# Kernel optimization log

Measured on AMD Instinct MI355X. Metric: run time of the kernel, lower is better.

## Reference

```python
import jax, jax.numpy as jnp
import numpy as np

N_NODES = 50000
N_EDGES = 800000
IN_FEAT = 128
INTER_DIM = 128
OUT_FEAT = 128
EDGE_W_DIM = 3


def setup_inputs() -> dict:
    key = jax.random.key(0)
    ks = jax.random.split(key, 8)
    h = jax.random.normal(ks[0], (N_NODES, IN_FEAT), dtype=jnp.float32)
    edge_src = jax.random.randint(ks[1], (N_EDGES,), 0, N_NODES, dtype=jnp.int32)
    edge_dst = jax.random.randint(ks[2], (N_EDGES,), 0, N_NODES, dtype=jnp.int32)
    edge_w = jax.random.normal(ks[3], (N_EDGES, EDGE_W_DIM), dtype=jnp.float32)
    # xavier-normal-ish init, gain for relu
    gain = float(np.sqrt(2.0))
    W1 = jax.random.normal(ks[4], (INTER_DIM, IN_FEAT + EDGE_W_DIM), dtype=jnp.float32)
    W1 = W1 * (gain * np.sqrt(2.0 / (INTER_DIM + IN_FEAT + EDGE_W_DIM)))
    b1 = jnp.zeros((INTER_DIM,), dtype=jnp.float32)
    W2 = jax.random.normal(ks[5], (OUT_FEAT, IN_FEAT + INTER_DIM), dtype=jnp.float32)
    W2 = W2 * (gain * np.sqrt(2.0 / (OUT_FEAT + IN_FEAT + INTER_DIM)))
    b2 = jnp.zeros((OUT_FEAT,), dtype=jnp.float32)
    return {"h": h, "edge_src": edge_src, "edge_dst": edge_dst, "edge_w": edge_w,
            "W1": W1, "b1": b1, "W2": W2, "b2": b2}


def reference(h, edge_src, edge_dst, edge_w, W1, b1, W2, b2):
    n_nodes = h.shape[0]
    # per-edge message: concat(src node feature, edge weight) -> [E, in_feat+3]
    m = jnp.concatenate([h[edge_src], edge_w], axis=1)
    # linear1 + leaky_relu (torch default negative_slope=0.01)
    tmp = m @ W1.T + b1  # [E, inter_dim]
    tmp = jnp.where(tmp >= 0, tmp, 0.01 * tmp)
    # mean over incoming edges per destination node; zero-in-degree nodes get 0
    sums = jax.ops.segment_sum(tmp, edge_dst, num_segments=n_nodes)
    counts = jax.ops.segment_sum(jnp.ones((tmp.shape[0],), dtype=tmp.dtype),
                                 edge_dst, num_segments=n_nodes)
    h_N = sums / jnp.maximum(counts, 1.0)[:, None]  # [N, inter_dim]
    # tail: concat + linear2 + relu
    h_total = jnp.concatenate([h, h_N], axis=1)  # [N, in_feat+inter_dim]
    return jax.nn.relu(h_total @ W2.T + b2)
```

## Files before the change

kernel.cpp:

```cpp
#include <hip/hip_runtime.h>
#include <hip/hip_bf16.h>

#define N_NODES 50000
#define N_EDGES 800000
#define N_TILES 3125
#define CSR_BLOCKS 782
#define PROJ_BLOCKS 782
#define BUCKET_CAP 64

typedef __attribute__((ext_vector_type(8))) short short8;
typedef __attribute__((ext_vector_type(4))) float f32x4;
typedef __attribute__((ext_vector_type(2))) float fl2;

#define OFF_G     0
#define OFF_CUR   1600000
#define OFF_BKT   6400000
#define OFF_W1BP  12866384
#define OFF_BP1   12866896
#define OFF_BP2   12875088

__device__ inline unsigned bf16rne(float f) {
    unsigned u = __float_as_uint(f);
    return (u + 0x7fffu + ((u >> 16) & 1u)) >> 16;
}
__device__ inline unsigned pk2(float lo, float hi) {
    return bf16rne(lo) | (bf16rne(hi) << 16);
}
union FragU { unsigned u[4]; short8 s; uint4 v; };

template <bool HI>
__device__ inline fl2 fp8x2_dec_w(unsigned s) {
#if __has_builtin(__builtin_amdgcn_cvt_pk_f32_fp8)
    return __builtin_amdgcn_cvt_pk_f32_fp8((int)s, HI);
#else
    unsigned v = HI ? (s >> 16) : s;
    fl2 r;
    unsigned lo = v & 0xffu, h2 = (v >> 8) & 0xffu;
    unsigned blo = ((lo & 0x80u) << 24) | ((lo & 0x7fu) << 20);
    unsigned bhi = ((h2 & 0x80u) << 24) | ((h2 & 0x7fu) << 20);
    r.x = __uint_as_float(blo) * 0x1p120f;
    r.y = __uint_as_float(bhi) * 0x1p120f;
    return r;
#endif
}
__device__ inline unsigned fp8x4_enc(float a, float b, float c, float d) {
#if __has_builtin(__builtin_amdgcn_cvt_pk_fp8_f32)
    int u = __builtin_amdgcn_cvt_pk_fp8_f32(a, b, 0, false);
    u = __builtin_amdgcn_cvt_pk_fp8_f32(c, d, u, true);
    return (unsigned)u;
#else
    auto enc1 = [](float f) -> unsigned {
        unsigned u = __float_as_uint(f);
        unsigned sg = (u >> 24) & 0x80u;
        float af = fabsf(f);
        if (af < 0x1p-6f) return sg;
        if (af >= 448.f) return sg | 0x7eu;
        unsigned v = __float_as_uint(af);
        unsigned r = v + 0xFFFFFu + ((v >> 20) & 1u);
        unsigned E = r >> 23, m = (r >> 20) & 7u;
        return sg | ((E - 120u) << 3) | m;
    };
    return enc1(a) | (enc1(b) << 8) | (enc1(c) << 16) | (enc1(d) << 24);
#endif
}

__global__ __launch_bounds__(256) void repack_zero_kernel(
        const float* __restrict__ W1, const float* __restrict__ b1,
        const float* __restrict__ W2, float* __restrict__ W1bp,
        uint4* __restrict__ Bpack1, uint4* __restrict__ Bpack2,
        int* __restrict__ cursor) {
    int tid = blockIdx.x * 256 + threadIdx.x;
    if (tid < 2048) {
        int lane = tid & 63, ent = tid >> 6;
        int n = (ent & 7) * 16 + (lane & 15);
        int k0 = (ent >> 3) * 32 + ((lane >> 4) << 3);
        const float* src = W1 + n * 131 + k0;
        FragU f;
        f.u[0] = pk2(src[0], src[1]);
        f.u[1] = pk2(src[2], src[3]);
        f.u[2] = pk2(src[4], src[5]);
        f.u[3] = pk2(src[6], src[7]);
        Bpack1[ent * 64 + lane] = f.v;
    } else if (tid < 6144) {
        int t2 = tid - 2048;
        int lane = t2 & 63, ent = t2 >> 6;
        int n = (ent & 7) * 16 + (lane & 15);
        int k0 = (ent >> 3) * 32 + ((lane >> 4) << 3);
        const float* src = W2 + n * 256 + k0;
        FragU f;
        f.u[0] = pk2(src[0], src[1]);
        f.u[1] = pk2(src[2], src[3]);
        f.u[2] = pk2(src[4], src[5]);
        f.u[3] = pk2(src[6], src[7]);
        Bpack2[ent * 64 + lane] = f.v;
    }
    if (tid < 128) {
        W1bp[tid * 4 + 0] = W1[tid * 131 + 128];
        W1bp[tid * 4 + 1] = W1[tid * 131 + 129];
        W1bp[tid * 4 + 2] = W1[tid * 131 + 130];
        W1bp[tid * 4 + 3] = b1[tid];
    }
    if (tid < N_NODES) cursor[tid] = 0;
}

__global__ __launch_bounds__(256) void fused_bucket_proj(
        const int* __restrict__ esrc, const int* __restrict__ edst,
        const float* __restrict__ ew, int* __restrict__ cursor,
        uint2* __restrict__ bkt,
        const float* __restrict__ h, const uint4* __restrict__ Bpack1,
        unsigned* __restrict__ g8) {
    __shared__ float lds[64][132];
    const int role = blockIdx.x & 1;
    const int gb = blockIdx.x >> 1;

    if (role == 0) {
        const int base = gb * 1024 + threadIdx.x;
        int dst[4], src[4];
        float w0[4], w1[4], w2[4];
        bool ok[4];
        #pragma unroll
        for (int j = 0; j < 4; j++) {
            int e = base + j * 256;
            ok[j] = e < N_EDGES;
            int ce = ok[j] ? e : 0;
            dst[j] = edst[ce];
            src[j] = esrc[ce];
            w0[j] = ew[ce * 3 + 0];
            w1[j] = ew[ce * 3 + 1];
            w2[j] = ew[ce * 3 + 2];
        }
        int pos[4];
        #pragma unroll
        for (int j = 0; j < 4; j++)
            pos[j] = ok[j] ? atomicAdd(&cursor[dst[j]], 1) : BUCKET_CAP;
        #pragma unroll
        for (int j = 0; j < 4; j++) {
            if (ok[j] && pos[j] < BUCKET_CAP) {
                uint2 rec;
                rec.x = (unsigned)src[j] | (bf16rne(w0[j]) << 16);
                rec.y = bf16rne(w1[j]) | (bf16rne(w2[j]) << 16);
                bkt[(dst[j] << 6) + pos[j]] = rec;
            }
        }
        return;
    }

    const int wave = threadIdx.x >> 6;
    const int lane = threadIdx.x & 63;
    const int T = gb * 4 + wave;

    if (T < N_TILES) {
        f32x4 acc[8];
        #pragma unroll
        for (int i = 0; i < 8; i++) acc[i] = (f32x4)(0.f);

        const int row = T * 16 + (lane & 15);
        const float* hrow = h + row * 128 + ((lane >> 4) << 3);

        #pragma unroll
        for (int kt = 0; kt < 4; kt++) {
            float4 x0 = *(const float4*)(hrow + kt * 32);
            float4 x1 = *(const float4*)(hrow + kt * 32 + 4);
            FragU a;
            a.u[0] = pk2(x0.x, x0.y);
            a.u[1] = pk2(x0.z, x0.w);
            a.u[2] = pk2(x1.x, x1.y);
            a.u[3] = pk2(x1.z, x1.w);
            #pragma unroll
            for (int nt = 0; nt < 8; nt++) {
                FragU b;
                b.v = Bpack1[(kt * 8 + nt) * 64 + lane];
                acc[nt] = __builtin_amdgcn_mfma_f32_16x16x32_bf16(a.s, b.s, acc[nt], 0, 0, 0);
            }
        }
        #pragma unroll
        for (int nt = 0; nt < 8; nt++) {
            #pragma unroll
            for (int reg = 0; reg < 4; reg++) {
                int r = ((lane >> 4) << 2) + reg;
                lds[wave * 16 + r][nt * 16 + (lane & 15)] = acc[nt][reg];
            }
        }
    }
    __syncthreads();

    const int t = threadIdx.x;
    const int nodeL = t >> 2, seg = t & 3;
    const int gnode = gb * 64 + nodeL;
    if (gnode < N_NODES) {
        #pragma unroll
        for (int i = 0; i < 2; i++) {
            const float* p = &lds[nodeL][seg * 32 + i * 16];
            uint4 o;
            o.x = fp8x4_enc(p[0],  p[1],  p[2],  p[3]);
            o.y = fp8x4_enc(p[4],  p[5],  p[6],  p[7]);
            o.z = fp8x4_enc(p[8],  p[9],  p[10], p[11]);
            o.w = fp8x4_enc(p[12], p[13], p[14], p[15]);
            ((uint4*)g8)[gnode * 8 + seg * 2 + i] = o;
        }
    }
}

#define AGG_P 4
__global__ __launch_bounds__(256) void agg_final(
        const unsigned* __restrict__ g8u, const uint2* __restrict__ bkt,
        const int* __restrict__ cursor, const float* __restrict__ W1bp,
        const float* __restrict__ h, const uint4* __restrict__ Bpack2,
        const float* __restrict__ b2, float* __restrict__ out) {
    __shared__ __align__(16) unsigned ldsN[16 * 64];
    const int wave = threadIdx.x >> 6;
    const int lane = threadIdx.x & 63;
    const int half = lane >> 5;
    const int c = lane & 31;
    const int T = blockIdx.x;

    const float4 w0 = ((const float4*)W1bp)[4 * c + 0];
    const float4 w1 = ((const float4*)W1bp)[4 * c + 1];
    const float4 w2 = ((const float4*)W1bp)[4 * c + 2];
    const float4 w3 = ((const float4*)W1bp)[4 * c + 3];
    const fl2 cx0 = {w0.x, w1.x}, cx1 = {w2.x, w3.x};
    const fl2 cy0 = {w0.y, w1.y}, cy1 = {w2.y, w3.y};
    const fl2 cz0 = {w0.z, w1.z}, cz1 = {w2.z, w3.z};
    const fl2 cb0 = {w0.w, w1.w}, cb1 = {w2.w, w3.w};
    const fl2 kP = (fl2)(0.505f);
    const fl2 kA = (fl2)(0.495f);

    const int v0 = T * 16 + wave * 4;
    int degT4[4];
    uint2 rec[4];
    #pragma unroll
    for (int nl = 0; nl < 4; nl++) {
        degT4[nl] = cursor[v0 + nl];
        rec[nl] = bkt[((v0 + nl) << 6) + lane];
    }

#define EDGE_BODY(RX, RY, GV, SP, SA)                                                  \
    do {                                                                               \
        fl2 ry = (fl2)(__uint_as_float((RX) & 0xffff0000u));                           \
        fl2 rz = (fl2)(__uint_as_float((RY) << 16));                                   \
        fl2 rw = (fl2)(__uint_as_float((RY) & 0xffff0000u));                           \
        fl2 t0 = fp8x2_dec_w<false>(GV) + cb0;                                         \
        t0 = __builtin_elementwise_fma(cx0, ry, t0);                                   \
        t0 = __builtin_elementwise_fma(cy0, rz, t0);                                   \
        t0 = __builtin_elementwise_fma(cz0, rw, t0);                                   \
        acc0 = __builtin_elementwise_fma(SP, t0, acc0);                                \
        acc0 = __builtin_elementwise_fma(SA, __builtin_elementwise_abs(t0), acc0);     \
        fl2 t1 = fp8x2_dec_w<true>(GV) + cb1;                                          \
        t1 = __builtin_elementwise_fma(cx1, ry, t1);                                   \
        t1 = __builtin_elementwise_fma(cy1, rz, t1);                                   \
        t1 = __builtin_elementwise_fma(cz1, rw, t1);                                   \
        acc1 = __builtin_elementwise_fma(SP, t1, acc1);                                \
        acc1 = __builtin_elementwise_fma(SA, __builtin_elementwise_abs(t1), acc1);     \
    } while (0)

    #pragma unroll
    for (int nl = 0; nl < 4; nl++) {
        const int n = wave * 4 + nl;
        const int degT = degT4[nl];
        const int deg = (degT < BUCKET_CAP) ? degT : BUCKET_CAP;
        const uint2 myrec = rec[nl];
        fl2 acc0 = (fl2)(0.f), acc1 = (fl2)(0.f);

        const int npairs = deg >> 1;
        int j = 0;
        for (; j + AGG_P <= npairs; j += AGG_P) {
            unsigned rx[AGG_P], ryy[AGG_P];
            #pragma unroll
            for (int u = 0; u < AGG_P; u++) {
                const int idx = 2 * (j + u) + half;
                rx[u]  = __shfl(myrec.x, idx);
                ryy[u] = __shfl(myrec.y, idx);
            }
            unsigned gv[AGG_P];
            #pragma unroll
            for (int u = 0; u < AGG_P; u++) gv[u] = g8u[(rx[u] & 0xffffu) * 32 + c];
            #pragma unroll
            for (int u = 0; u < AGG_P; u++) EDGE_BODY(rx[u], ryy[u], gv[u], kP, kA);
        }
        for (; j < npairs; ++j) {
            const int idx = 2 * j + half;
            unsigned rx  = __shfl(myrec.x, idx);
            unsigned ryy = __shfl(myrec.y, idx);
            unsigned gv = g8u[(rx & 0xffffu) * 32 + c];
            EDGE_BODY(rx, ryy, gv, kP, kA);
        }
        if (deg & 1) {
            const float sc = (half == 0) ? 1.f : 0.f;
            const fl2 sP = (fl2)(0.505f * sc), sA = (fl2)(0.495f * sc);
            const int idx = deg - 1;
            unsigned rx  = __shfl(myrec.x, idx);
            unsigned ryy = __shfl(myrec.y, idx);
            unsigned gv = g8u[(rx & 0xffffu) * 32 + c];
            EDGE_BODY(rx, ryy, gv, sP, sA);
        }

        acc0.x += __shfl_xor(acc0.x, 32);
        acc0.y += __shfl_xor(acc0.y, 32);
        acc1.x += __shfl_xor(acc1.x, 32);
        acc1.y += __shfl_xor(acc1.y, 32);
        if (half == 0) {
            float inv = 1.0f / (float)((degT > 0) ? degT : 1);
            uint2 p;
            p.x = pk2(acc0.x * inv, acc0.y * inv);
            p.y = pk2(acc1.x * inv, acc1.y * inv);
            const int idx = (2 * c) ^ ((n & 7) << 2);
            *(uint2*)&ldsN[n * 64 + idx] = p;
        }
    }
#undef EDGE_BODY
    __syncthreads();

    f32x4 acc[2];
    acc[0] = (f32x4)(0.f);
    acc[1] = (f32x4)(0.f);

    const int row = T * 16 + (lane & 15);
    const int koff = (lane >> 4) << 3;
    const float* hrow = h + row * 128 + koff;

    #pragma unroll
    for (int kt = 0; kt < 8; kt++) {
        FragU a;
        if (kt < 4) {
            float4 x0 = *(const float4*)(hrow + kt * 32);
            float4 x1 = *(const float4*)(hrow + kt * 32 + 4);
            a.u[0] = pk2(x0.x, x0.y);
            a.u[1] = pk2(x0.z, x0.w);
            a.u[2] = pk2(x1.x, x1.y);
            a.u[3] = pk2(x1.z, x1.w);
        } else {
            const int nn = lane & 15;
            const int idx = (((kt - 4) << 4) + (koff >> 1)) ^ ((nn & 7) << 2);
            a.v = *(const uint4*)&ldsN[nn * 64 + idx];
        }
        #pragma unroll
        for (int j = 0; j < 2; j++) {
            const int nt = wave * 2 + j;
            FragU b;
            b.v = Bpack2[(kt * 8 + nt) * 64 + lane];
            acc[j] = __builtin_amdgcn_mfma_f32_16x16x32_bf16(a.s, b.s, acc[j], 0, 0, 0);
        }
    }
    #pragma unroll
    for (int j = 0; j < 2; j++) {
        const int nt = wave * 2 + j;
        const int ch = nt * 16 + (lane & 15);
        const float bias = b2[ch];
        #pragma unroll
        for (int reg = 0; reg < 4; reg++) {
            const int node = T * 16 + ((lane >> 4) << 2) + reg;
            out[node * 128 + ch] = fmaxf(acc[j][reg] + bias, 0.f);
        }
    }
}

extern "C" void kernel_launch(void* const* d_in, const int* in_sizes, int n_in,
                              void* d_out, int out_size, void* d_ws, size_t ws_size,
                              hipStream_t stream) {
    const float* h    = (const float*)d_in[0];
    const int*   esrc = (const int*)d_in[1];
    const int*   edst = (const int*)d_in[2];
    const float* ew   = (const float*)d_in[3];
    const float* W1   = (const float*)d_in[4];
    const float* b1   = (const float*)d_in[5];
    const float* W2   = (const float*)d_in[6];
    const float* b2   = (const float*)d_in[7];
    float* out = (float*)d_out;
    float* ws  = (float*)d_ws;

    unsigned* g8  = (unsigned*)(ws + OFF_G);
    int* cursor   = (int*)(ws + OFF_CUR);
    float* W1bp   = ws + OFF_W1BP;
    uint4* Bpack1 = (uint4*)(ws + OFF_BP1);
    uint4* Bpack2 = (uint4*)(ws + OFF_BP2);
    uint2* bkt    = (uint2*)(ws + OFF_BKT);

    repack_zero_kernel<<<196, 256, 0, stream>>>(W1, b1, W2, W1bp, Bpack1, Bpack2, cursor);

    fused_bucket_proj<<<CSR_BLOCKS + PROJ_BLOCKS, 256, 0, stream>>>(
        esrc, edst, ew, cursor, bkt, h, Bpack1, g8);

    agg_final<<<N_TILES, 256, 0, stream>>>(g8, bkt, cursor, W1bp, h, Bpack2, b2, out);
}
```

Baseline: 181.4 us.

## Use 8 waves per tile in agg_final with max-based leaky ReLU and 8-edge batching

Doubles the agg_final block to 512 threads, so each wave aggregates 2 destination nodes instead of 4 and computes one 16-column MFMA output tile instead of two. The leaky ReLU becomes max(t, 0.01t) instead of two FMAs on t and |t|. The edge loop now issues 8 gathers per batch and uses a predicated masked tail instead of separate pair and odd-edge paths. The aim is more memory-level parallelism per CU and shorter per-wave latency chains, at the cost of more waves per block and wasted lanes in the padded tail.

Result: slower. 207.3 us (+14.3%).

```diff
diff --git a/kernel.cpp b/kernel.cpp
--- a/kernel.cpp
+++ b/kernel.cpp
@@ -201,8 +201,7 @@
     }
 }
 
-#define AGG_P 4
-__global__ __launch_bounds__(256) void agg_final(
+__global__ __launch_bounds__(512) void agg_final(
         const unsigned* __restrict__ g8u, const uint2* __restrict__ bkt,
         const int* __restrict__ cursor, const float* __restrict__ W1bp,
         const float* __restrict__ h, const uint4* __restrict__ Bpack2,
@@ -222,19 +221,19 @@
     const fl2 cy0 = {w0.y, w1.y}, cy1 = {w2.y, w3.y};
     const fl2 cz0 = {w0.z, w1.z}, cz1 = {w2.z, w3.z};
     const fl2 cb0 = {w0.w, w1.w}, cb1 = {w2.w, w3.w};
-    const fl2 kP = (fl2)(0.505f);
-    const fl2 kA = (fl2)(0.495f);
-
-    const int v0 = T * 16 + wave * 4;
-    int degT4[4];
-    uint2 rec[4];
+    const fl2 kSlope = (fl2)(0.01f);
+    const fl2 kOne = (fl2)(1.0f);
+
+    const int v0 = T * 16 + wave * 2;
+    int degT2[2];
+    uint2 rec[2];
     #pragma unroll
-    for (int nl = 0; nl < 4; nl++) {
-        degT4[nl] = cursor[v0 + nl];
+    for (int nl = 0; nl < 2; nl++) {
+        degT2[nl] = cursor[v0 + nl];
         rec[nl] = bkt[((v0 + nl) << 6) + lane];
     }
 
-#define EDGE_BODY(RX, RY, GV, SP, SA)                                                  \
+#define EDGE_BODY(RX, RY, GV, S2)                                                      \
     do {                                                                               \
         fl2 ry = (fl2)(__uint_as_float((RX) & 0xffff0000u));                           \
         fl2 rz = (fl2)(__uint_as_float((RY) << 16));                                   \
@@ -243,55 +242,57 @@
         t0 = __builtin_elementwise_fma(cx0, ry, t0);                                   \
         t0 = __builtin_elementwise_fma(cy0, rz, t0);                                   \
         t0 = __builtin_elementwise_fma(cz0, rw, t0);                                   \
-        acc0 = __builtin_elementwise_fma(SP, t0, acc0);                                \
-        acc0 = __builtin_elementwise_fma(SA, __builtin_elementwise_abs(t0), acc0);     \
+        fl2 m0 = __builtin_elementwise_max(t0, t0 * kSlope);                           \
+        acc0 = __builtin_elementwise_fma(S2, m0, acc0);                                \
         fl2 t1 = fp8x2_dec_w<true>(GV) + cb1;                                          \
         t1 = __builtin_elementwise_fma(cx1, ry, t1);                                   \
         t1 = __builtin_elementwise_fma(cy1, rz, t1);                                   \
         t1 = __builtin_elementwise_fma(cz1, rw, t1);                                   \
-        acc1 = __builtin_elementwise_fma(SP, t1, acc1);                                \
-        acc1 = __builtin_elementwise_fma(SA, __builtin_elementwise_abs(t1), acc1);     \
+        fl2 m1 = __builtin_elementwise_max(t1, t1 * kSlope);                           \
+        acc1 = __builtin_elementwise_fma(S2, m1, acc1);                                \
     } while (0)
 
     #pragma unroll
-    for (int nl = 0; nl < 4; nl++) {
-        const int n = wave * 4 + nl;
-        const int degT = degT4[nl];
+    for (int nl = 0; nl < 2; nl++) {
+        const int n = wave * 2 + nl;
+        const int degT = degT2[nl];
         const int deg = (degT < BUCKET_CAP) ? degT : BUCKET_CAP;
         const uint2 myrec = rec[nl];
         fl2 acc0 = (fl2)(0.f), acc1 = (fl2)(0.f);
 
-        const int npairs = deg >> 1;
-        int j = 0;
-        for (; j + AGG_P <= npairs; j += AGG_P) {
-            unsigned rx[AGG_P], ryy[AGG_P];
-            #pragma unroll
-            for (int u = 0; u < AGG_P; u++) {
-                const int idx = 2 * (j + u) + half;
-                rx[u]  = __shfl(myrec.x, idx);
-                ryy[u] = __shfl(myrec.y, idx);
-            }
-            unsigned gv[AGG_P];
-            #pragma unroll
-            for (int u = 0; u < AGG_P; u++) gv[u] = g8u[(rx[u] & 0xffffu) * 32 + c];
-            #pragma unroll
-            for (int u = 0; u < AGG_P; u++) EDGE_BODY(rx[u], ryy[u], gv[u], kP, kA);
-        }
-        for (; j < npairs; ++j) {
-            const int idx = 2 * j + half;
-            unsigned rx  = __shfl(myrec.x, idx);
-            unsigned ryy = __shfl(myrec.y, idx);
-            unsigned gv = g8u[(rx & 0xffffu) * 32 + c];
-            EDGE_BODY(rx, ryy, gv, kP, kA);
-        }
-        if (deg & 1) {
-            const float sc = (half == 0) ? 1.f : 0.f;
-            const fl2 sP = (fl2)(0.505f * sc), sA = (fl2)(0.495f * sc);
-            const int idx = deg - 1;
-            unsigned rx  = __shfl(myrec.x, idx);
-            unsigned ryy = __shfl(myrec.y, idx);
-            unsigned gv = g8u[(rx & 0xffffu) * 32 + c];
-            EDGE_BODY(rx, ryy, gv, sP, sA);
+        int j0 = 0;
+        for (; j0 + 16 <= deg; j0 += 16) {
+            unsigned rxh[8], ryy[8], gv[8];
+            #pragma unroll
+            for (int u = 0; u < 8; u++) {
+                const int e = j0 + 2 * u + half;
+                unsigned rx = __shfl(myrec.x, e);
+                ryy[u] = __shfl(myrec.y, e);
+                gv[u] = g8u[(rx & 0xffffu) * 32 + c];
+                rxh[u] = rx;
+            }
+            #pragma unroll
+            for (int u = 0; u < 8; u++) EDGE_BODY(rxh[u], ryy[u], gv[u], kOne);
+        }
+        if (j0 < deg) {
+            unsigned rxh[8], ryy[8], gv[8];
+            float scv[8];
+            #pragma unroll
+            for (int u = 0; u < 8; u++) {
+                const int e = j0 + 2 * u + half;
+                const bool oke = e < deg;
+                const int idxe = oke ? e : 0;
+                unsigned rx = __shfl(myrec.x, idxe);
+                ryy[u] = __shfl(myrec.y, idxe);
+                gv[u] = g8u[(rx & 0xffffu) * 32 + c];
+                rxh[u] = rx;
+                scv[u] = oke ? 1.f : 0.f;
+            }
+            #pragma unroll
+            for (int u = 0; u < 8; u++) {
+                const fl2 s2 = (fl2)(scv[u]);
+                EDGE_BODY(rxh[u], ryy[u], gv[u], s2);
+            }
         }
 
         acc0.x += __shfl_xor(acc0.x, 32);
@@ -310,9 +311,7 @@
 #undef EDGE_BODY
     __syncthreads();
 
-    f32x4 acc[2];
-    acc[0] = (f32x4)(0.f);
-    acc[1] = (f32x4)(0.f);
+    f32x4 acc = (f32x4)(0.f);
 
     const int row = T * 16 + (lane & 15);
     const int koff = (lane >> 4) << 3;
@@ -333,23 +332,17 @@
             const int idx = (((kt - 4) << 4) + (koff >> 1)) ^ ((nn & 7) << 2);
             a.v = *(const uint4*)&ldsN[nn * 64 + idx];
         }
-        #pragma unroll
-        for (int j = 0; j < 2; j++) {
-            const int nt = wave * 2 + j;
-            FragU b;
-            b.v = Bpack2[(kt * 8 + nt) * 64 + lane];
-            acc[j] = __builtin_amdgcn_mfma_f32_16x16x32_bf16(a.s, b.s, acc[j], 0, 0, 0);
-        }
-    }
-    #pragma unroll
-    for (int j = 0; j < 2; j++) {
-        const int nt = wave * 2 + j;
-        const int ch = nt * 16 + (lane & 15);
+        FragU b;
+        b.v = Bpack2[(kt * 8 + wave) * 64 + lane];
+        acc = __builtin_amdgcn_mfma_f32_16x16x32_bf16(a.s, b.s, acc, 0, 0, 0);
+    }
+    {
+        const int ch = wave * 16 + (lane & 15);
         const float bias = b2[ch];
         #pragma unroll
         for (int reg = 0; reg < 4; reg++) {
             const int node = T * 16 + ((lane >> 4) << 2) + reg;
-            out[node * 128 + ch] = fmaxf(acc[j][reg] + bias, 0.f);
+            out[node * 128 + ch] = fmaxf(acc[reg] + bias, 0.f);
         }
     }
 }
@@ -380,5 +373,5 @@
     fused_bucket_proj<<<CSR_BLOCKS + PROJ_BLOCKS, 256, 0, stream>>>(
         esrc, edst, ew, cursor, bkt, h, Bpack1, g8);
 
-    agg_final<<<N_TILES, 256, 0, stream>>>(g8, bkt, cursor, W1bp, h, Bpack2, b2, out);
-}
+    agg_final<<<N_TILES, 512, 0, stream>>>(g8, bkt, cursor, W1bp, h, Bpack2, b2, out);
+}
```

## Split projected features into two channel halves and process four edges per wave step

Applied to the files above, without the earlier changes.

The projected fp8 node features are stored as two separate 64-channel halves, so each edge gather in the aggregation kernel touches a 64-byte row segment instead of 128 bytes. The aggregation loop runs twice, once per half, with 16 lanes per edge and 4 edges in flight per wave step, masking edges past the degree instead of using a separate odd-edge tail. Leaky-ReLU becomes max(t, 0.01t) instead of the abs-based blend. In exchange, the edge records and shuffles are repeated for each half, an extra cross-lane reduction stage is added, and masked lanes do wasted work on nodes whose degree is not a multiple of four.

Measured after the change: 194.5 us. +7.2%, slower.

```diff
diff --git a/kernel.cpp b/kernel.cpp
--- a/kernel.cpp
+++ b/kernel.cpp
@@ -13,6 +13,7 @@
 typedef __attribute__((ext_vector_type(2))) float fl2;
 
 #define OFF_G     0
+#define G_HALF    800000
 #define OFF_CUR   1600000
 #define OFF_BKT   6400000
 #define OFF_W1BP  12866384
@@ -188,6 +189,7 @@
     const int nodeL = t >> 2, seg = t & 3;
     const int gnode = gb * 64 + nodeL;
     if (gnode < N_NODES) {
+        unsigned* dst = g8 + ((seg < 2) ? 0 : G_HALF) + gnode * 16 + (seg & 1) * 8;
         #pragma unroll
         for (int i = 0; i < 2; i++) {
             const float* p = &lds[nodeL][seg * 32 + i * 16];
@@ -196,12 +198,11 @@
             o.y = fp8x4_enc(p[4],  p[5],  p[6],  p[7]);
             o.z = fp8x4_enc(p[8],  p[9],  p[10], p[11]);
             o.w = fp8x4_enc(p[12], p[13], p[14], p[15]);
-            ((uint4*)g8)[gnode * 8 + seg * 2 + i] = o;
-        }
-    }
-}
-
-#define AGG_P 4
+            ((uint4*)dst)[i] = o;
+        }
+    }
+}
+
 __global__ __launch_bounds__(256) void agg_final(
         const unsigned* __restrict__ g8u, const uint2* __restrict__ bkt,
         const int* __restrict__ cursor, const float* __restrict__ W1bp,
@@ -210,20 +211,9 @@
     __shared__ __align__(16) unsigned ldsN[16 * 64];
     const int wave = threadIdx.x >> 6;
     const int lane = threadIdx.x & 63;
-    const int half = lane >> 5;
-    const int c = lane & 31;
+    const int c16 = lane & 15;
+    const int esub = lane >> 4;
     const int T = blockIdx.x;
-
-    const float4 w0 = ((const float4*)W1bp)[4 * c + 0];
-    const float4 w1 = ((const float4*)W1bp)[4 * c + 1];
-    const float4 w2 = ((const float4*)W1bp)[4 * c + 2];
-    const float4 w3 = ((const float4*)W1bp)[4 * c + 3];
-    const fl2 cx0 = {w0.x, w1.x}, cx1 = {w2.x, w3.x};
-    const fl2 cy0 = {w0.y, w1.y}, cy1 = {w2.y, w3.y};
-    const fl2 cz0 = {w0.z, w1.z}, cz1 = {w2.z, w3.z};
-    const fl2 cb0 = {w0.w, w1.w}, cb1 = {w2.w, w3.w};
-    const fl2 kP = (fl2)(0.505f);
-    const fl2 kA = (fl2)(0.495f);
 
     const int v0 = T * 16 + wave * 4;
     int degT4[4];
@@ -234,7 +224,7 @@
         rec[nl] = bkt[((v0 + nl) << 6) + lane];
     }
 
-#define EDGE_BODY(RX, RY, GV, SP, SA)                                                  \
+#define EDGE_BODY(RX, RY, GV, MK)                                                      \
     do {                                                                               \
         fl2 ry = (fl2)(__uint_as_float((RX) & 0xffff0000u));                           \
         fl2 rz = (fl2)(__uint_as_float((RY) << 16));                                   \
@@ -243,71 +233,89 @@
         t0 = __builtin_elementwise_fma(cx0, ry, t0);                                   \
         t0 = __builtin_elementwise_fma(cy0, rz, t0);                                   \
         t0 = __builtin_elementwise_fma(cz0, rw, t0);                                   \
-        acc0 = __builtin_elementwise_fma(SP, t0, acc0);                                \
-        acc0 = __builtin_elementwise_fma(SA, __builtin_elementwise_abs(t0), acc0);     \
+        fl2 l0 = __builtin_elementwise_max(t0, t0 * kSlope);                           \
+        acc0 = __builtin_elementwise_fma(MK, l0, acc0);                                \
         fl2 t1 = fp8x2_dec_w<true>(GV) + cb1;                                          \
         t1 = __builtin_elementwise_fma(cx1, ry, t1);                                   \
         t1 = __builtin_elementwise_fma(cy1, rz, t1);                                   \
         t1 = __builtin_elementwise_fma(cz1, rw, t1);                                   \
-        acc1 = __builtin_elementwise_fma(SP, t1, acc1);                                \
-        acc1 = __builtin_elementwise_fma(SA, __builtin_elementwise_abs(t1), acc1);     \
+        fl2 l1 = __builtin_elementwise_max(t1, t1 * kSlope);                           \
+        acc1 = __builtin_elementwise_fma(MK, l1, acc1);                                \
     } while (0)
 
+#define SLOT_LOADS(S, U)                                                               \
+    do {                                                                               \
+        const int eidx = 4 * (S) + esub;                                               \
+        rxh[U] = __shfl(myrec.x, eidx);                                                \
+        ryy[U] = __shfl(myrec.y, eidx);                                                \
+        gv[U] = gp[(rxh[U] & 0xffffu) * 16 + c16];                                     \
+        mk[U] = (eidx < deg) ? 1.f : 0.f;                                              \
+    } while (0)
+
+    const fl2 kSlope = (fl2)(0.01f);
+
     #pragma unroll
-    for (int nl = 0; nl < 4; nl++) {
-        const int n = wave * 4 + nl;
-        const int degT = degT4[nl];
-        const int deg = (degT < BUCKET_CAP) ? degT : BUCKET_CAP;
-        const uint2 myrec = rec[nl];
-        fl2 acc0 = (fl2)(0.f), acc1 = (fl2)(0.f);
-
-        const int npairs = deg >> 1;
-        int j = 0;
-        for (; j + AGG_P <= npairs; j += AGG_P) {
-            unsigned rx[AGG_P], ryy[AGG_P];
-            #pragma unroll
-            for (int u = 0; u < AGG_P; u++) {
-                const int idx = 2 * (j + u) + half;
-                rx[u]  = __shfl(myrec.x, idx);
-                ryy[u] = __shfl(myrec.y, idx);
-            }
-            unsigned gv[AGG_P];
-            #pragma unroll
-            for (int u = 0; u < AGG_P; u++) gv[u] = g8u[(rx[u] & 0xffffu) * 32 + c];
-            #pragma unroll
-            for (int u = 0; u < AGG_P; u++) EDGE_BODY(rx[u], ryy[u], gv[u], kP, kA);
-        }
-        for (; j < npairs; ++j) {
-            const int idx = 2 * j + half;
-            unsigned rx  = __shfl(myrec.x, idx);
-            unsigned ryy = __shfl(myrec.y, idx);
-            unsigned gv = g8u[(rx & 0xffffu) * 32 + c];
-            EDGE_BODY(rx, ryy, gv, kP, kA);
-        }
-        if (deg & 1) {
-            const float sc = (half == 0) ? 1.f : 0.f;
-            const fl2 sP = (fl2)(0.505f * sc), sA = (fl2)(0.495f * sc);
-            const int idx = deg - 1;
-            unsigned rx  = __shfl(myrec.x, idx);
-            unsigned ryy = __shfl(myrec.y, idx);
-            unsigned gv = g8u[(rx & 0xffffu) * 32 + c];
-            EDGE_BODY(rx, ryy, gv, sP, sA);
-        }
-
-        acc0.x += __shfl_xor(acc0.x, 32);
-        acc0.y += __shfl_xor(acc0.y, 32);
-        acc1.x += __shfl_xor(acc1.x, 32);
-        acc1.y += __shfl_xor(acc1.y, 32);
-        if (half == 0) {
-            float inv = 1.0f / (float)((degT > 0) ? degT : 1);
-            uint2 p;
-            p.x = pk2(acc0.x * inv, acc0.y * inv);
-            p.y = pk2(acc1.x * inv, acc1.y * inv);
-            const int idx = (2 * c) ^ ((n & 7) << 2);
-            *(uint2*)&ldsN[n * 64 + idx] = p;
+    for (int p = 0; p < 2; ++p) {
+        const unsigned* gp = g8u + p * G_HALF;
+        const int chb = (p << 6) + (c16 << 2);
+        const float4 w0 = ((const float4*)W1bp)[chb + 0];
+        const float4 w1 = ((const float4*)W1bp)[chb + 1];
+        const float4 w2 = ((const float4*)W1bp)[chb + 2];
+        const float4 w3 = ((const float4*)W1bp)[chb + 3];
+        const fl2 cx0 = {w0.x, w1.x}, cx1 = {w2.x, w3.x};
+        const fl2 cy0 = {w0.y, w1.y}, cy1 = {w2.y, w3.y};
+        const fl2 cz0 = {w0.z, w1.z}, cz1 = {w2.z, w3.z};
+        const fl2 cb0 = {w0.w, w1.w}, cb1 = {w2.w, w3.w};
+
+        #pragma unroll
+        for (int nl = 0; nl < 4; nl++) {
+            const int n = wave * 4 + nl;
+            const int degT = degT4[nl];
+            const int deg = (degT < BUCKET_CAP) ? degT : BUCKET_CAP;
+            const uint2 myrec = rec[nl];
+            const int nslots = (deg + 3) >> 2;
+            fl2 acc0 = (fl2)(0.f), acc1 = (fl2)(0.f);
+
+            int s = 0;
+            for (; s + 4 <= nslots; s += 4) {
+                unsigned rxh[4], ryy[4], gv[4];
+                float mk[4];
+                #pragma unroll
+                for (int u = 0; u < 4; u++) SLOT_LOADS(s + u, u);
+                #pragma unroll
+                for (int u = 0; u < 4; u++) {
+                    const fl2 m2 = (fl2)(mk[u]);
+                    EDGE_BODY(rxh[u], ryy[u], gv[u], m2);
+                }
+            }
+            for (; s < nslots; ++s) {
+                unsigned rxh[1], ryy[1], gv[1];
+                float mk[1];
+                SLOT_LOADS(s, 0);
+                const fl2 m2 = (fl2)(mk[0]);
+                EDGE_BODY(rxh[0], ryy[0], gv[0], m2);
+            }
+
+            acc0.x += __shfl_xor(acc0.x, 16);
+            acc0.y += __shfl_xor(acc0.y, 16);
+            acc1.x += __shfl_xor(acc1.x, 16);
+            acc1.y += __shfl_xor(acc1.y, 16);
+            acc0.x += __shfl_xor(acc0.x, 32);
+            acc0.y += __shfl_xor(acc0.y, 32);
+            acc1.x += __shfl_xor(acc1.x, 32);
+            acc1.y += __shfl_xor(acc1.y, 32);
+            if (lane < 16) {
+                float inv = 1.0f / (float)((degT > 0) ? degT : 1);
+                uint2 pp;
+                pp.x = pk2(acc0.x * inv, acc0.y * inv);
+                pp.y = pk2(acc1.x * inv, acc1.y * inv);
+                const int idx = ((p << 5) + 2 * c16) ^ ((n & 7) << 2);
+                *(uint2*)&ldsN[n * 64 + idx] = pp;
+            }
         }
     }
 #undef EDGE_BODY
+#undef SLOT_LOADS
     __syncthreads();
 
     f32x4 acc[2];
```
